# Kernel optimization log

Measured on AMD Instinct MI355X. Metric: run time of the kernel, lower is better.

The kernel has to match this reference:

```python
import jax, jax.numpy as jnp
import numpy as np

ALPHA = 0.25  # sparsity init kwarg


def setup_inputs() -> dict:
    key = jax.random.key(0)
    x = jax.random.uniform(key, (32, 256, 256, 16), dtype=jnp.float32)
    return {"x": x}


def reference(x):
    # Original TF code loops over every pixel i in H*W, slicing (B,1,C) and
    # calling force_sparsity, where p = reduce_mean over the WHOLE slice
    # (batch AND channel). Vectorized: p has shape (H, W).
    p = jnp.mean(x, axis=(0, 3))            # (H, W) per-pixel mean over B,C
    p_b = p[None, :, :, None]                # broadcast to (1, H, W, 1)
    beta = (1.0 - ALPHA) / (1.0 - p_b)
    le = p_b >= ALPHA                        # branch selector per pixel
    out = jnp.where(le,
                    x * ALPHA / p_b,
                    1.0 - beta * (1.0 - x))
    return out
```

## Files before the change

### kernel.cpp

```cpp
#include <hip/hip_runtime.h>


#define ALPHA 0.25f

typedef float v4f __attribute__((ext_vector_type(4)));

__global__ __launch_bounds__(256) void reduce_kernel(
    const float* __restrict__ x, float2* __restrict__ ad) {
  constexpr long ELEM_PER_B = 1L << 20;

  const int t  = blockIdx.x * 256 + threadIdx.x;
  const int hw = t >> 3;
  const int cq = t & 3;
  const int bh = (t >> 2) & 1;

  const float* base = x + (long)hw * 16 + cq * 4 + (long)bh * 16 * ELEM_PER_B;

  float s = 0.0f;
#pragma unroll
  for (int bi = 0; bi < 16; ++bi) {
    const float4 v = *(const float4*)(base + (long)bi * ELEM_PER_B);
    s += (v.x + v.y) + (v.z + v.w);
  }
  s += __shfl_xor(s, 1);
  s += __shfl_xor(s, 2);
  s += __shfl_xor(s, 4);
  const float p = s * (1.0f / 512.0f);

  float a, d;
  if (p >= ALPHA) {
    a = ALPHA / p;
    d = 0.0f;
  } else {
    const float beta = (1.0f - ALPHA) / (1.0f - p);
    a = beta;
    d = 1.0f - beta;
  }
  if ((t & 7) == 0) ad[hw] = make_float2(a, d);
}

__global__ __launch_bounds__(256) void apply_kernel(
    const float* __restrict__ x, const float2* __restrict__ ad,
    float* __restrict__ out) {
  constexpr long STRIDE_F4 = 2048L * 256;
  constexpr int F4_PER_B_MASK = (1 << 18) - 1;

  const long i = (long)blockIdx.x * 256 + threadIdx.x;
  const int inb = (int)i & F4_PER_B_MASK;
  const float2 adv = ad[inb >> 2];

  const float4* __restrict__ xp = (const float4*)x + i;
  v4f* __restrict__ op = (v4f*)out + i;

#pragma unroll
  for (int j = 0; j < 16; ++j) {
    const float4 v = xp[j * STRIDE_F4];
    v4f r;
    r.x = fmaf(adv.x, v.x, adv.y);
    r.y = fmaf(adv.x, v.y, adv.y);
    r.z = fmaf(adv.x, v.z, adv.y);
    r.w = fmaf(adv.x, v.w, adv.y);
    __builtin_nontemporal_store(r, op + j * STRIDE_F4);
  }
}

extern "C" void kernel_launch(void* const* d_in, const int* in_sizes, int n_in,
                              void* d_out, int out_size, void* d_ws, size_t ws_size,
                              hipStream_t stream) {
  const float* x = (const float*)d_in[0];
  float* out = (float*)d_out;
  float2* ad = (float2*)d_ws;

  reduce_kernel<<<dim3(2048), dim3(256), 0, stream>>>(x, ad);
  apply_kernel<<<dim3(2048), dim3(256), 0, stream>>>(x, ad, out);
}
```

Before: 252.8 us.

## Fuse reduction and apply kernels, keeping x in registers

Merges the per-pixel mean reduction and the affine apply into one kernel. Each thread keeps its 16 loaded float4 values in registers and, after the shuffle reduction, writes the output directly. This removes the second full read of x, the workspace round-trip and one kernel launch. The cost is higher register pressure per thread, which may lower occupancy.

```diff
diff --git a/kernel.cpp b/kernel.cpp
--- a/kernel.cpp
+++ b/kernel.cpp
@@ -5,8 +5,8 @@
 
 typedef float v4f __attribute__((ext_vector_type(4)));
 
-__global__ __launch_bounds__(256) void reduce_kernel(
-    const float* __restrict__ x, float2* __restrict__ ad) {
+__global__ __launch_bounds__(256, 4) void fused_kernel(
+    const float* __restrict__ x, float* __restrict__ out) {
   constexpr long ELEM_PER_B = 1L << 20;
 
   const int t  = blockIdx.x * 256 + threadIdx.x;
@@ -14,14 +14,22 @@
   const int cq = t & 3;
   const int bh = (t >> 2) & 1;
 
-  const float* base = x + (long)hw * 16 + cq * 4 + (long)bh * 16 * ELEM_PER_B;
+  const long off = (long)hw * 16 + cq * 4 + (long)bh * 16 * ELEM_PER_B;
+  const float* __restrict__ xp = x + off;
 
+  float4 v[16];
   float s = 0.0f;
 #pragma unroll
   for (int bi = 0; bi < 16; ++bi) {
-    const float4 v = *(const float4*)(base + (long)bi * ELEM_PER_B);
-    s += (v.x + v.y) + (v.z + v.w);
+    v[bi] = *(const float4*)(xp + (long)bi * ELEM_PER_B);
+    s += (v[bi].x + v[bi].y) + (v[bi].z + v[bi].w);
   }
+#pragma unroll
+  for (int bi = 0; bi < 16; ++bi) {
+    asm volatile("" : "+v"(v[bi].x), "+v"(v[bi].y), "+v"(v[bi].z),
+                      "+v"(v[bi].w));
+  }
+
   s += __shfl_xor(s, 1);
   s += __shfl_xor(s, 2);
   s += __shfl_xor(s, 4);
@@ -36,31 +44,16 @@
     a = beta;
     d = 1.0f - beta;
   }
-  if ((t & 7) == 0) ad[hw] = make_float2(a, d);
-}
 
-__global__ __launch_bounds__(256) void apply_kernel(
-    const float* __restrict__ x, const float2* __restrict__ ad,
-    float* __restrict__ out) {
-  constexpr long STRIDE_F4 = 2048L * 256;
-  constexpr int F4_PER_B_MASK = (1 << 18) - 1;
-
-  const long i = (long)blockIdx.x * 256 + threadIdx.x;
-  const int inb = (int)i & F4_PER_B_MASK;
-  const float2 adv = ad[inb >> 2];
-
-  const float4* __restrict__ xp = (const float4*)x + i;
-  v4f* __restrict__ op = (v4f*)out + i;
-
+  float* __restrict__ op = out + off;
 #pragma unroll
-  for (int j = 0; j < 16; ++j) {
-    const float4 v = xp[j * STRIDE_F4];
+  for (int bi = 0; bi < 16; ++bi) {
     v4f r;
-    r.x = fmaf(adv.x, v.x, adv.y);
-    r.y = fmaf(adv.x, v.y, adv.y);
-    r.z = fmaf(adv.x, v.z, adv.y);
-    r.w = fmaf(adv.x, v.w, adv.y);
-    __builtin_nontemporal_store(r, op + j * STRIDE_F4);
+    r.x = fmaf(a, v[bi].x, d);
+    r.y = fmaf(a, v[bi].y, d);
+    r.z = fmaf(a, v[bi].z, d);
+    r.w = fmaf(a, v[bi].w, d);
+    __builtin_nontemporal_store(r, (v4f*)(op + (long)bi * ELEM_PER_B));
   }
 }
 
@@ -69,8 +62,5 @@
                               hipStream_t stream) {
   const float* x = (const float*)d_in[0];
   float* out = (float*)d_out;
-  float2* ad = (float2*)d_ws;
-
-  reduce_kernel<<<dim3(2048), dim3(256), 0, stream>>>(x, ad);
-  apply_kernel<<<dim3(2048), dim3(256), 0, stream>>>(x, ad, out);
+  fused_kernel<<<dim3(2048), dim3(256), 0, stream>>>(x, out);
 }
```

Result: faster. 243.7 us (-3.6%).

## Split reduction into per-batch partial sums and contiguous-per-thread apply pass

Applied to the files above, without the earlier changes.

Replaces the strided cross-batch reduction with a kernel where each thread reads 64 contiguous floats and writes per-batch per-pixel channel sums to workspace, followed by a small finalize kernel that sums over batch and computes the affine coefficients. The apply kernel now processes 16 contiguous float4s per thread using four per-pixel coefficient pairs, and uses normal stores instead of nontemporal ones. The aim is sequential memory streams in place of widely strided access, at the cost of an extra launch, an 8 MB partial-sum round trip, and per-thread accesses strided by 256 bytes across lanes, which may coalesce less well.

```diff
diff --git a/kernel.cpp b/kernel.cpp
--- a/kernel.cpp
+++ b/kernel.cpp
@@ -5,28 +5,37 @@
 
 typedef float v4f __attribute__((ext_vector_type(4)));
 
-__global__ __launch_bounds__(256) void reduce_kernel(
-    const float* __restrict__ x, float2* __restrict__ ad) {
-  constexpr long ELEM_PER_B = 1L << 20;
+__global__ __launch_bounds__(256) void reduce_part_kernel(
+    const float* __restrict__ x, float* __restrict__ p_part) {
+  const long fbase = (long)blockIdx.x * 16384 + threadIdx.x * 64;
+  const float4* __restrict__ xp = (const float4*)(x + fbase);
 
-  const int t  = blockIdx.x * 256 + threadIdx.x;
-  const int hw = t >> 3;
-  const int cq = t & 3;
-  const int bh = (t >> 2) & 1;
+  float cs[4];
+#pragma unroll
+  for (int k = 0; k < 4; ++k) {
+    float s = 0.0f;
+#pragma unroll
+    for (int j = 0; j < 4; ++j) {
+      const float4 v = xp[4 * k + j];
+      s += (v.x + v.y) + (v.z + v.w);
+    }
+    cs[k] = s;
+  }
+  const int b  = blockIdx.x >> 6;
+  const int hw = ((blockIdx.x & 63) << 10) + (threadIdx.x << 2);
+  v4f o = {cs[0], cs[1], cs[2], cs[3]};
+  *(v4f*)(p_part + (long)b * 65536 + hw) = o;
+}
 
-  const float* base = x + (long)hw * 16 + cq * 4 + (long)bh * 16 * ELEM_PER_B;
-
+__global__ __launch_bounds__(256) void finalize_kernel(
+    const float* __restrict__ p_part, float2* __restrict__ ad) {
+  const int hw = blockIdx.x * 256 + threadIdx.x;
   float s = 0.0f;
 #pragma unroll
-  for (int bi = 0; bi < 16; ++bi) {
-    const float4 v = *(const float4*)(base + (long)bi * ELEM_PER_B);
-    s += (v.x + v.y) + (v.z + v.w);
+  for (int b = 0; b < 32; ++b) {
+    s += p_part[(long)b * 65536 + hw];
   }
-  s += __shfl_xor(s, 1);
-  s += __shfl_xor(s, 2);
-  s += __shfl_xor(s, 4);
   const float p = s * (1.0f / 512.0f);
-
   float a, d;
   if (p >= ALPHA) {
     a = ALPHA / p;
@@ -36,31 +45,34 @@
     a = beta;
     d = 1.0f - beta;
   }
-  if ((t & 7) == 0) ad[hw] = make_float2(a, d);
+  ad[hw] = make_float2(a, d);
 }
 
 __global__ __launch_bounds__(256) void apply_kernel(
     const float* __restrict__ x, const float2* __restrict__ ad,
     float* __restrict__ out) {
-  constexpr long STRIDE_F4 = 2048L * 256;
-  constexpr int F4_PER_B_MASK = (1 << 18) - 1;
+  const long g = (long)blockIdx.x * 256 + threadIdx.x;
+  const long f4base = g * 16;
+  const int  inb = (int)f4base & ((1 << 18) - 1);
+  const int  hw0 = inb >> 2;
 
-  const long i = (long)blockIdx.x * 256 + threadIdx.x;
-  const int inb = (int)i & F4_PER_B_MASK;
-  const float2 adv = ad[inb >> 2];
+  float2 t[4];
+#pragma unroll
+  for (int k = 0; k < 4; ++k) t[k] = ad[hw0 + k];
 
-  const float4* __restrict__ xp = (const float4*)x + i;
-  v4f* __restrict__ op = (v4f*)out + i;
-
+  const float4* __restrict__ xp = (const float4*)x + f4base;
+  v4f* __restrict__ op = (v4f*)out + f4base;
 #pragma unroll
   for (int j = 0; j < 16; ++j) {
-    const float4 v = xp[j * STRIDE_F4];
+    const float4 v = xp[j];
+    const float a = t[j >> 2].x;
+    const float d = t[j >> 2].y;
     v4f r;
-    r.x = fmaf(adv.x, v.x, adv.y);
-    r.y = fmaf(adv.x, v.y, adv.y);
-    r.z = fmaf(adv.x, v.z, adv.y);
-    r.w = fmaf(adv.x, v.w, adv.y);
-    __builtin_nontemporal_store(r, op + j * STRIDE_F4);
+    r.x = fmaf(a, v.x, d);
+    r.y = fmaf(a, v.y, d);
+    r.z = fmaf(a, v.z, d);
+    r.w = fmaf(a, v.w, d);
+    op[j] = r;
   }
 }
 
@@ -69,8 +81,10 @@
                               hipStream_t stream) {
   const float* x = (const float*)d_in[0];
   float* out = (float*)d_out;
-  float2* ad = (float2*)d_ws;
+  float*  p_part = (float*)d_ws;
+  float2* ad     = (float2*)((char*)d_ws + 32L * 65536 * 4);
 
-  reduce_kernel<<<dim3(2048), dim3(256), 0, stream>>>(x, ad);
-  apply_kernel<<<dim3(2048), dim3(256), 0, stream>>>(x, ad, out);
+  reduce_part_kernel<<<dim3(2048), dim3(256), 0, stream>>>(x, p_part);
+  finalize_kernel  <<<dim3(256),  dim3(256), 0, stream>>>(p_part, ad);
+  apply_kernel     <<<dim3(2048), dim3(256), 0, stream>>>(x, ad, out);
 }
```

Measured after the change: 269.6 us. 1.07x slower.
